# Kernel optimization log

Hardware: AMD Instinct MI355X
Metric: run time of the kernel (lower is better)

The kernel has to match this reference:

```python
import math
import jax, jax.numpy as jnp
import numpy as np

B, N, M, C, H, POS = 2, 2048, 64, 256, 8, 6
D = C // H  # head_dim = 32
SCALE = 1.0 / math.sqrt(D)
LAMDA = 1.0


def setup_inputs() -> dict:
    key = jax.random.key(0)
    ks = jax.random.split(key, 15)
    s = 0.05
    return {
        "pairwise_g": jax.random.normal(ks[0], (B, N, N, POS), jnp.float32),
        "coset_functions": jax.random.normal(ks[1], (B, N, C), jnp.float32),
        "mask": jnp.ones((B, N), dtype=bool),
        "Wq": jax.random.normal(ks[2], (C, C), jnp.float32) * s,
        "bq": jax.random.normal(ks[3], (C,), jnp.float32) * s,
        "Wk": jax.random.normal(ks[4], (C, C), jnp.float32) * s,
        "bk": jax.random.normal(ks[5], (C,), jnp.float32) * s,
        "Wl": jax.random.normal(ks[6], (C, POS), jnp.float32) * s,
        "bl": jax.random.normal(ks[7], (C,), jnp.float32) * s,
        "u": jax.random.normal(ks[8], (H, D), jnp.float32) * s,
        "v": jax.random.normal(ks[9], (H, D), jnp.float32) * s,
        "Wi": jax.random.normal(ks[10], (C, C), jnp.float32) * s,
        "bi": jax.random.normal(ks[11], (C,), jnp.float32) * s,
        "Wo": jax.random.normal(ks[12], (C, C), jnp.float32) * s,
        "bo": jax.random.normal(ks[13], (C,), jnp.float32) * s,
    }


def reference(pairwise_g, coset_functions, mask, Wq, bq, Wk, bk, Wl, bl, u, v, Wi, bi, Wo, bo):
    # ---- extract_neighbourhoods (mc_samples=M, fill=1.0 -> k == k_ball, permutation irrelevant)
    dists = jnp.linalg.norm(pairwise_g, axis=-1)                      # (B,N,N)
    dists = jnp.where(mask[:, None, :], dists, jnp.float32(1e8))
    _, nbhd_idx = jax.lax.top_k(-dists, M)                            # (B,N,M) nearest neighbors
    nbhd_pg = jnp.take_along_axis(pairwise_g, nbhd_idx[..., None], axis=2)  # (B,N,M,POS)
    gather_rows = jax.vmap(lambda arr, ix: arr[ix])                   # gather along point axis per batch
    nbhd_cf = gather_rows(coset_functions, nbhd_idx)                  # (B,N,M,C)
    nbhd_mask = gather_rows(mask, nbhd_idx)                           # (B,N,M)

    # ---- RelativePositionKernel
    Q = (coset_functions @ Wq.T + bq).reshape(B, N, H, D).transpose(0, 2, 1, 3)  # (B,H,N,D)
    K = (coset_functions @ Wk.T + bk).reshape(B, N, H, D).transpose(0, 2, 1, 3)  # (B,H,N,D)
    e = (nbhd_pg @ Wl.T + bl).reshape(B, N, M, H, D)                  # (B,N,M,H,D)

    S = jnp.einsum('bhnd,bhkd->bhnk', Q, K)                           # dense scores (as original)
    Sg = jnp.take_along_axis(S, nbhd_idx[:, None, :, :], axis=3)      # (B,H,N,M)
    e_term = jnp.einsum('bnmhd,bhnd->bhnm', e, Q + v[None, :, None, :])
    uK = jnp.einsum('hd,bhkd->bhk', u, K)                             # (B,H,N)
    uKg = jnp.take_along_axis(uK[:, :, None, :], nbhd_idx[:, None, :, :], axis=3)  # (B,H,N,M)
    A = (Sg + LAMDA * e_term + uKg) * SCALE
    A = A.transpose(0, 2, 3, 1)                                       # (B,N,M,H)

    # ---- masked softmax over neighbors
    A = jnp.where(nbhd_mask[..., None], A, jnp.float32(-1e38))
    attn = jax.nn.softmax(A, axis=2)                                  # (B,N,M,H)

    # ---- value projection + weighted sum + output linear
    Vv = (nbhd_cf @ Wi.T + bi).reshape(B, N, M, H, D)                 # (B,N,M,H,D)
    out = jnp.einsum('bnmh,bnmhd->bnhd', attn, Vv).reshape(B, N, C)
    out = out @ Wo.T + bo                                             # (B,N,c_out)
    return out
```

## Files before the change

kernel.cpp:

```cpp
#include <hip/hip_runtime.h>
#include <stdint.h>

#define NB 2
#define NN 2048
#define MM 64
#define CC 256
#define HH 8
#define DD 32
#define PP 6
#define ATT_SCALE 0.17677669529663687f

typedef __attribute__((ext_vector_type(8))) short short8;
typedef __attribute__((ext_vector_type(4))) float f32x4;

__device__ __forceinline__ uint16_t f2bf(float f) {
  union { float f; uint32_t u; } c; c.f = f;
  return (uint16_t)((c.u + 0x7fffu + ((c.u >> 16) & 1u)) >> 16);
}
__device__ __forceinline__ float blo(uint32_t u) {
  union { uint32_t u; float f; } c; c.u = u << 16; return c.f;
}
__device__ __forceinline__ float bhi(uint32_t u) {
  union { uint32_t u; float f; } c; c.u = u & 0xffff0000u; return c.f;
}
__device__ __forceinline__ short8 pack8(float4 a, float4 b) {
  short8 r;
  r[0] = (short)f2bf(a.x); r[1] = (short)f2bf(a.y);
  r[2] = (short)f2bf(a.z); r[3] = (short)f2bf(a.w);
  r[4] = (short)f2bf(b.x); r[5] = (short)f2bf(b.y);
  r[6] = (short)f2bf(b.z); r[7] = (short)f2bf(b.w);
  return r;
}

__global__ __launch_bounds__(256) void k_select(const float* __restrict__ pg,
                                                int* __restrict__ nidx) {
  const int row = blockIdx.x;
  const int t = threadIdx.x;
  const int wave = t >> 6;
  const int lane = t & 63;

  __shared__ float s_mn[4], s_mx[4];
  __shared__ uint32_t s_hist[256];
  __shared__ uint32_t s_scan[256];
  __shared__ float s_cd[NN];
  __shared__ int   s_cj[NN];
  __shared__ int s_tbin;
  __shared__ uint32_t s_c0;
  __shared__ int s_cw;
  __shared__ int s_ct;

  if (t < MM) nidx[(size_t)row * MM + t] = t;

  const float4* base = (const float4*)(pg + (size_t)row * NN * PP);

  float d[8];
  float mn = 3.4e38f, mx = -3.4e38f;
#pragma unroll
  for (int i = 0; i < 4; i++) {
    const int j0 = i * 512 + 2 * t;
    const float4 qa = base[(size_t)(j0 >> 1) * 3 + 0];
    const float4 qb = base[(size_t)(j0 >> 1) * 3 + 1];
    const float4 qc = base[(size_t)(j0 >> 1) * 3 + 2];
    float s0 = __fmul_rn(qa.x, qa.x);
    s0 = __fadd_rn(s0, __fmul_rn(qa.y, qa.y));
    s0 = __fadd_rn(s0, __fmul_rn(qa.z, qa.z));
    s0 = __fadd_rn(s0, __fmul_rn(qa.w, qa.w));
    s0 = __fadd_rn(s0, __fmul_rn(qb.x, qb.x));
    s0 = __fadd_rn(s0, __fmul_rn(qb.y, qb.y));
    float s1 = __fmul_rn(qb.z, qb.z);
    s1 = __fadd_rn(s1, __fmul_rn(qb.w, qb.w));
    s1 = __fadd_rn(s1, __fmul_rn(qc.x, qc.x));
    s1 = __fadd_rn(s1, __fmul_rn(qc.y, qc.y));
    s1 = __fadd_rn(s1, __fmul_rn(qc.z, qc.z));
    s1 = __fadd_rn(s1, __fmul_rn(qc.w, qc.w));
    const float d0 = __fsqrt_rn(s0);
    const float d1 = __fsqrt_rn(s1);
    d[2 * i] = d0; d[2 * i + 1] = d1;
    mn = fminf(mn, fminf(d0, d1));
    mx = fmaxf(mx, fmaxf(d0, d1));
  }

#pragma unroll
  for (int off = 32; off; off >>= 1) {
    mn = fminf(mn, __shfl_xor(mn, off));
    mx = fmaxf(mx, __shfl_xor(mx, off));
  }
  if (lane == 0) { s_mn[wave] = mn; s_mx[wave] = mx; }
  s_hist[t] = 0;
  __syncthreads();
  mn = fminf(fminf(s_mn[0], s_mn[1]), fminf(s_mn[2], s_mn[3]));
  mx = fmaxf(fmaxf(s_mx[0], s_mx[1]), fmaxf(s_mx[2], s_mx[3]));
  const float range = mx - mn;
  const float scale = (range > 0.f) ? (256.0f / range) : 0.f;

  int bins[8];
#pragma unroll
  for (int i = 0; i < 8; i++) {
    int bn = (int)((d[i] - mn) * scale);
    bn = (bn > 255) ? 255 : (bn < 0 ? 0 : bn);
    bins[i] = bn;
    atomicAdd(&s_hist[bn], 1u);
  }
  __syncthreads();

  s_scan[t] = s_hist[t];
  __syncthreads();
  for (int off = 1; off < 256; off <<= 1) {
    const uint32_t add = (t >= off) ? s_scan[t - off] : 0u;
    __syncthreads();
    s_scan[t] += add;
    __syncthreads();
  }

  if (t == 0) { s_cw = 0; s_ct = 0; }
  if (s_scan[t] >= (uint32_t)MM && (t == 0 || s_scan[t - 1] < (uint32_t)MM)) {
    s_tbin = t;
    s_c0 = (t == 0) ? 0u : s_scan[t - 1];
  }
  __syncthreads();

  const int tbin = s_tbin;
  const int c0 = (int)s_c0;

#pragma unroll
  for (int i = 0; i < 8; i++) {
    const int j = (i >> 1) * 512 + 2 * t + (i & 1);
    if (bins[i] < tbin) {
      const int pos = atomicAdd(&s_cw, 1);
      if (pos < MM) nidx[(size_t)row * MM + pos] = j;
    } else if (bins[i] == tbin) {
      const int pos = atomicAdd(&s_ct, 1);
      s_cd[pos] = d[i];
      s_cj[pos] = j;
    }
  }
  __syncthreads();

  if (t < 64) {
    const int cnt = s_ct;
    const int r = MM - c0;
    for (int it = 0; it < r; ++it) {
      float bd = 3.4e38f; int bj = 0x7fffffff; int bi = -1;
      for (int i = t; i < cnt; i += 64) {
        const float dd = s_cd[i]; const int jj = s_cj[i];
        if (dd < bd || (dd == bd && jj < bj)) { bd = dd; bj = jj; bi = i; }
      }
#pragma unroll
      for (int off = 32; off; off >>= 1) {
        const float od = __shfl_xor(bd, off);
        const int oj = __shfl_xor(bj, off);
        const int oi = __shfl_xor(bi, off);
        if (od < bd || (od == bd && oj < bj)) { bd = od; bj = oj; bi = oi; }
      }
      if (t == 0 && bi >= 0) {
        s_cd[bi] = 3.4e38f;
        nidx[(size_t)row * MM + c0 + it] = bj;
      }
      __threadfence_block();
    }
  }
}

__global__ __launch_bounds__(64) void k_gemm_qkv(
    const float* __restrict__ A,
    const float* __restrict__ W0, const float* __restrict__ W1, const float* __restrict__ W2,
    const float* __restrict__ b0, const float* __restrict__ b1, const float* __restrict__ b2,
    float* __restrict__ Qo, uint16_t* __restrict__ Ko, uint16_t* __restrict__ Vo) {
  const int z = blockIdx.z;
  const float* W = (z == 0) ? W0 : ((z == 1) ? W1 : W2);
  const float* bias = (z == 0) ? b0 : ((z == 1) ? b1 : b2);

  const int lane = threadIdx.x;
  const int m = lane & 15;
  const int quad = lane >> 4;
  const int row0 = blockIdx.x * 16;
  const int c0 = blockIdx.y * 64;

  f32x4 acc0 = {0.f, 0.f, 0.f, 0.f};
  f32x4 acc1 = {0.f, 0.f, 0.f, 0.f};
  f32x4 acc2 = {0.f, 0.f, 0.f, 0.f};
  f32x4 acc3 = {0.f, 0.f, 0.f, 0.f};

#pragma unroll
  for (int k0 = 0; k0 < CC; k0 += 32) {
    const float4* ap = (const float4*)(A + (size_t)(row0 + m) * CC + k0 + quad * 8);
    const float4* bp0 = (const float4*)(W + (size_t)(c0 + 0 + m) * CC + k0 + quad * 8);
    const float4* bp1 = (const float4*)(W + (size_t)(c0 + 16 + m) * CC + k0 + quad * 8);
    const float4* bp2 = (const float4*)(W + (size_t)(c0 + 32 + m) * CC + k0 + quad * 8);
    const float4* bp3 = (const float4*)(W + (size_t)(c0 + 48 + m) * CC + k0 + quad * 8);
    const short8 a = pack8(ap[0], ap[1]);
    const short8 f0 = pack8(bp0[0], bp0[1]);
    const short8 f1 = pack8(bp1[0], bp1[1]);
    const short8 f2 = pack8(bp2[0], bp2[1]);
    const short8 f3 = pack8(bp3[0], bp3[1]);
    acc0 = __builtin_amdgcn_mfma_f32_16x16x32_bf16(a, f0, acc0, 0, 0, 0);
    acc1 = __builtin_amdgcn_mfma_f32_16x16x32_bf16(a, f1, acc1, 0, 0, 0);
    acc2 = __builtin_amdgcn_mfma_f32_16x16x32_bf16(a, f2, acc2, 0, 0, 0);
    acc3 = __builtin_amdgcn_mfma_f32_16x16x32_bf16(a, f3, acc3, 0, 0, 0);
  }

  const int orow = row0 + quad * 4;
  f32x4 accs[4] = {acc0, acc1, acc2, acc3};
#pragma unroll
  for (int f = 0; f < 4; ++f) {
    const int col = c0 + f * 16 + m;
    const float bv = bias[col];
#pragma unroll
    for (int r = 0; r < 4; ++r) {
      const float val = accs[f][r] + bv;
      const size_t o = (size_t)(orow + r) * CC + col;
      if (z == 0) Qo[o] = val;
      else if (z == 1) Ko[o] = f2bf(val);
      else Vo[o] = f2bf(val);
    }
  }
}

__global__ __launch_bounds__(64) void k_gemm_out(const uint16_t* __restrict__ A,
                                                 const float* __restrict__ W,
                                                 const float* __restrict__ bias,
                                                 float* __restrict__ O) {
  const int lane = threadIdx.x;
  const int m = lane & 15;
  const int quad = lane >> 4;
  const int row0 = blockIdx.x * 16;
  const int c0 = blockIdx.y * 32;

  f32x4 acc0 = {0.f, 0.f, 0.f, 0.f};
  f32x4 acc1 = {0.f, 0.f, 0.f, 0.f};

#pragma unroll
  for (int k0 = 0; k0 < CC; k0 += 32) {
    const short8 a = *(const short8*)(A + (size_t)(row0 + m) * CC + k0 + quad * 8);
    const float4* bp0 = (const float4*)(W + (size_t)(c0 + 0 + m) * CC + k0 + quad * 8);
    const float4* bp1 = (const float4*)(W + (size_t)(c0 + 16 + m) * CC + k0 + quad * 8);
    const short8 f0 = pack8(bp0[0], bp0[1]);
    const short8 f1 = pack8(bp1[0], bp1[1]);
    acc0 = __builtin_amdgcn_mfma_f32_16x16x32_bf16(a, f0, acc0, 0, 0, 0);
    acc1 = __builtin_amdgcn_mfma_f32_16x16x32_bf16(a, f1, acc1, 0, 0, 0);
  }

  const int orow = row0 + quad * 4;
  f32x4 accs[2] = {acc0, acc1};
#pragma unroll
  for (int f = 0; f < 2; ++f) {
    const int col = c0 + f * 16 + m;
    const float bv = bias[col];
#pragma unroll
    for (int r = 0; r < 4; ++r) {
      O[(size_t)(orow + r) * CC + col] = accs[f][r] + bv;
    }
  }
}

__global__ __launch_bounds__(256) void k_attn(const float* __restrict__ pg,
                                              const int* __restrict__ nidx,
                                              const float* __restrict__ Q,
                                              const uint16_t* __restrict__ K,
                                              const uint16_t* __restrict__ V,
                                              const float* __restrict__ Wl,
                                              const float* __restrict__ bl,
                                              const float* __restrict__ u,
                                              const float* __restrict__ v,
                                              uint16_t* __restrict__ attnV) {
  const int row = blockIdx.x;
  const int b = row >> 11;
  const int t = threadIdx.x;
  const int wave = t >> 6;
  const int lane = t & 63;

  __shared__ int s_idx[MM];
  __shared__ float s_npg[MM][7];
  __shared__ float s_qu[CC];
  __shared__ float s_wt[HH][8];
  __shared__ float s_sc[HH][MM];
  __shared__ float s_part[CC];

  if (t < MM) s_idx[t] = nidx[(size_t)row * MM + t] & (NN - 1);
  const float qv_ = Q[(size_t)row * CC + t];
  s_qu[t] = qv_ + u[t];
  __syncthreads();

  if (t < MM) {
    const int jj = s_idx[t];
    const float2* p = (const float2*)(pg + ((size_t)row * NN + (size_t)jj) * PP);
    const float2 p0 = p[0], p1 = p[1], p2 = p[2];
    s_npg[t][0] = p0.x; s_npg[t][1] = p0.y;
    s_npg[t][2] = p1.x; s_npg[t][3] = p1.y;
    s_npg[t][4] = p2.x; s_npg[t][5] = p2.y;
  }

  {
    const int h = t >> 5;
    const float qpv = qv_ + v[t];
    float part[7];
#pragma unroll
    for (int p = 0; p < 6; p++) part[p] = Wl[(size_t)t * PP + p] * qpv;
    part[6] = bl[t] * qpv;
#pragma unroll
    for (int off = 1; off < 32; off <<= 1) {
#pragma unroll
      for (int p = 0; p < 7; p++) part[p] += __shfl_xor(part[p], off);
    }
    if ((t & 31) == 0) {
#pragma unroll
      for (int p = 0; p < 7; p++) s_wt[h][p] = part[p];
    }
  }
  __syncthreads();

#pragma unroll
  for (int pr = 0; pr < 2; ++pr) {
    const int h = wave + pr * 4;
    const int m = lane;
    const int kidx = s_idx[m];
    const uint4* kr = (const uint4*)(K + ((size_t)(b * NN + kidx)) * CC + h * DD);
    float acc = s_wt[h][6];
#pragma unroll
    for (int p = 0; p < 6; p++) acc += s_npg[m][p] * s_wt[h][p];
    const float* qu = &s_qu[h * DD];
    float a2 = 0.f;
#pragma unroll
    for (int w4 = 0; w4 < 4; w4++) {
      const uint4 kv = kr[w4];
      const float* q8 = qu + w4 * 8;
      a2 += q8[0] * blo(kv.x) + q8[1] * bhi(kv.x)
          + q8[2] * blo(kv.y) + q8[3] * bhi(kv.y)
          + q8[4] * blo(kv.z) + q8[5] * bhi(kv.z)
          + q8[6] * blo(kv.w) + q8[7] * bhi(kv.w);
    }
    s_sc[h][m] = (acc + a2) * ATT_SCALE;
  }
  __syncthreads();

#pragma unroll
  for (int pr = 0; pr < 2; ++pr) {
    const int h = wave + pr * 4;
    const float x = s_sc[h][lane];
    float mxv = x;
#pragma unroll
    for (int off = 32; off; off >>= 1) mxv = fmaxf(mxv, __shfl_xor(mxv, off));
    const float e = expf(x - mxv);
    float sm = e;
#pragma unroll
    for (int off = 32; off; off >>= 1) sm += __shfl_xor(sm, off);
    s_sc[h][lane] = e / sm;
  }
  __syncthreads();

  {
    const int h2 = t >> 7;
    const int ci = (t & 127) * 2;
    const int h = ci >> 5;
    const uint32_t* Vb32 = (const uint32_t*)(V + (size_t)b * NN * CC);
    float a0 = 0.f, a1 = 0.f;
#pragma unroll 8
    for (int m = h2; m < MM; m += 2) {
      const uint32_t pv = Vb32[(size_t)s_idx[m] * (CC / 2) + (ci >> 1)];
      const float p = s_sc[h][m];
      a0 += p * blo(pv);
      a1 += p * bhi(pv);
    }
    if (h2 == 1) { s_part[ci] = a0; s_part[ci + 1] = a1; }
    __syncthreads();
    if (h2 == 0) {
      attnV[(size_t)row * CC + ci]     = f2bf(a0 + s_part[ci]);
      attnV[(size_t)row * CC + ci + 1] = f2bf(a1 + s_part[ci + 1]);
    }
  }
}

extern "C" void kernel_launch(void* const* d_in, const int* in_sizes, int n_in,
                              void* d_out, int out_size, void* d_ws, size_t ws_size,
                              hipStream_t stream) {
  const float* pg = (const float*)d_in[0];
  const float* cf = (const float*)d_in[1];
  const float* Wq = (const float*)d_in[3];
  const float* bq = (const float*)d_in[4];
  const float* Wk = (const float*)d_in[5];
  const float* bk = (const float*)d_in[6];
  const float* Wl = (const float*)d_in[7];
  const float* bl = (const float*)d_in[8];
  const float* u  = (const float*)d_in[9];
  const float* v  = (const float*)d_in[10];
  const float* Wi = (const float*)d_in[11];
  const float* bi = (const float*)d_in[12];
  const float* Wo = (const float*)d_in[13];
  const float* bo = (const float*)d_in[14];

  char* ws = (char*)d_ws;
  int* nidx = (int*)ws;
  float* Q  = (float*)(ws + (size_t)1 * (1 << 20));
  uint16_t* K = (uint16_t*)(ws + (size_t)5 * (1 << 20));
  uint16_t* V = (uint16_t*)(ws + (size_t)7 * (1 << 20));
  uint16_t* aV = (uint16_t*)(ws + (size_t)9 * (1 << 20));
  float* out = (float*)d_out;

  hipLaunchKernelGGL(k_gemm_qkv, dim3(256, 4, 3), dim3(64), 0, stream,
                     cf, Wq, Wk, Wi, bq, bk, bi, Q, K, V);
  hipLaunchKernelGGL(k_select, dim3(NB * NN), dim3(256), 0, stream, pg, nidx);
  hipLaunchKernelGGL(k_attn, dim3(NB * NN), dim3(256), 0, stream,
                     pg, nidx, Q, K, V, Wl, bl, u, v, aV);
  hipLaunchKernelGGL(k_gemm_out, dim3(256, 8), dim3(64), 0, stream,
                     aV, Wo, bo, out);
}
```

Measured before the change: 384.1 us.

## Fuse neighbour selection into attention kernel and use wave-shuffle histogram scan

Merges the top-k neighbour selection kernel and the attention kernel into one per-row kernel, so neighbour indices stay in shared memory instead of being written to and re-read from global memory. This also removes one launch. The 256-bin histogram prefix sum is replaced by a wave-level shuffle scan plus a cross-wave add, which cuts the number of block barriers. The fused kernel uses more shared memory per block, which may reduce occupancy.

```diff
diff --git a/kernel.cpp b/kernel.cpp
--- a/kernel.cpp
+++ b/kernel.cpp
@@ -32,14 +32,115 @@
   return r;
 }
 
-__global__ __launch_bounds__(256) void k_select(const float* __restrict__ pg,
-                                                int* __restrict__ nidx) {
+__global__ __launch_bounds__(64) void k_gemm_qkv(
+    const float* __restrict__ A,
+    const float* __restrict__ W0, const float* __restrict__ W1, const float* __restrict__ W2,
+    const float* __restrict__ b0, const float* __restrict__ b1, const float* __restrict__ b2,
+    float* __restrict__ Qo, uint16_t* __restrict__ Ko, uint16_t* __restrict__ Vo) {
+  const int z = blockIdx.z;
+  const float* W = (z == 0) ? W0 : ((z == 1) ? W1 : W2);
+  const float* bias = (z == 0) ? b0 : ((z == 1) ? b1 : b2);
+
+  const int lane = threadIdx.x;
+  const int m = lane & 15;
+  const int quad = lane >> 4;
+  const int row0 = blockIdx.x * 16;
+  const int c0 = blockIdx.y * 64;
+
+  f32x4 acc0 = {0.f, 0.f, 0.f, 0.f};
+  f32x4 acc1 = {0.f, 0.f, 0.f, 0.f};
+  f32x4 acc2 = {0.f, 0.f, 0.f, 0.f};
+  f32x4 acc3 = {0.f, 0.f, 0.f, 0.f};
+
+#pragma unroll
+  for (int k0 = 0; k0 < CC; k0 += 32) {
+    const float4* ap = (const float4*)(A + (size_t)(row0 + m) * CC + k0 + quad * 8);
+    const float4* bp0 = (const float4*)(W + (size_t)(c0 + 0 + m) * CC + k0 + quad * 8);
+    const float4* bp1 = (const float4*)(W + (size_t)(c0 + 16 + m) * CC + k0 + quad * 8);
+    const float4* bp2 = (const float4*)(W + (size_t)(c0 + 32 + m) * CC + k0 + quad * 8);
+    const float4* bp3 = (const float4*)(W + (size_t)(c0 + 48 + m) * CC + k0 + quad * 8);
+    const short8 a = pack8(ap[0], ap[1]);
+    const short8 f0 = pack8(bp0[0], bp0[1]);
+    const short8 f1 = pack8(bp1[0], bp1[1]);
+    const short8 f2 = pack8(bp2[0], bp2[1]);
+    const short8 f3 = pack8(bp3[0], bp3[1]);
+    acc0 = __builtin_amdgcn_mfma_f32_16x16x32_bf16(a, f0, acc0, 0, 0, 0);
+    acc1 = __builtin_amdgcn_mfma_f32_16x16x32_bf16(a, f1, acc1, 0, 0, 0);
+    acc2 = __builtin_amdgcn_mfma_f32_16x16x32_bf16(a, f2, acc2, 0, 0, 0);
+    acc3 = __builtin_amdgcn_mfma_f32_16x16x32_bf16(a, f3, acc3, 0, 0, 0);
+  }
+
+  const int orow = row0 + quad * 4;
+  f32x4 accs[4] = {acc0, acc1, acc2, acc3};
+#pragma unroll
+  for (int f = 0; f < 4; ++f) {
+    const int col = c0 + f * 16 + m;
+    const float bv = bias[col];
+#pragma unroll
+    for (int r = 0; r < 4; ++r) {
+      const float val = accs[f][r] + bv;
+      const size_t o = (size_t)(orow + r) * CC + col;
+      if (z == 0) Qo[o] = val;
+      else if (z == 1) Ko[o] = f2bf(val);
+      else Vo[o] = f2bf(val);
+    }
+  }
+}
+
+__global__ __launch_bounds__(64) void k_gemm_out(const uint16_t* __restrict__ A,
+                                                 const float* __restrict__ W,
+                                                 const float* __restrict__ bias,
+                                                 float* __restrict__ O) {
+  const int lane = threadIdx.x;
+  const int m = lane & 15;
+  const int quad = lane >> 4;
+  const int row0 = blockIdx.x * 16;
+  const int c0 = blockIdx.y * 32;
+
+  f32x4 acc0 = {0.f, 0.f, 0.f, 0.f};
+  f32x4 acc1 = {0.f, 0.f, 0.f, 0.f};
+
+#pragma unroll
+  for (int k0 = 0; k0 < CC; k0 += 32) {
+    const short8 a = *(const short8*)(A + (size_t)(row0 + m) * CC + k0 + quad * 8);
+    const float4* bp0 = (const float4*)(W + (size_t)(c0 + 0 + m) * CC + k0 + quad * 8);
+    const float4* bp1 = (const float4*)(W + (size_t)(c0 + 16 + m) * CC + k0 + quad * 8);
+    const short8 f0 = pack8(bp0[0], bp0[1]);
+    const short8 f1 = pack8(bp1[0], bp1[1]);
+    acc0 = __builtin_amdgcn_mfma_f32_16x16x32_bf16(a, f0, acc0, 0, 0, 0);
+    acc1 = __builtin_amdgcn_mfma_f32_16x16x32_bf16(a, f1, acc1, 0, 0, 0);
+  }
+
+  const int orow = row0 + quad * 4;
+  f32x4 accs[2] = {acc0, acc1};
+#pragma unroll
+  for (int f = 0; f < 2; ++f) {
+    const int col = c0 + f * 16 + m;
+    const float bv = bias[col];
+#pragma unroll
+    for (int r = 0; r < 4; ++r) {
+      O[(size_t)(orow + r) * CC + col] = accs[f][r] + bv;
+    }
+  }
+}
+
+__global__ __launch_bounds__(256) void k_fused(const float* __restrict__ pg,
+                                               const float* __restrict__ Q,
+                                               const uint16_t* __restrict__ K,
+                                               const uint16_t* __restrict__ V,
+                                               const float* __restrict__ Wl,
+                                               const float* __restrict__ bl,
+                                               const float* __restrict__ u,
+                                               const float* __restrict__ v,
+                                               uint16_t* __restrict__ attnV) {
   const int row = blockIdx.x;
+  const int b = row >> 11;
   const int t = threadIdx.x;
   const int wave = t >> 6;
   const int lane = t & 63;
 
   __shared__ float s_mn[4], s_mx[4];
+  __shared__ uint32_t s_wsum[4];
   __shared__ uint32_t s_hist[256];
   __shared__ uint32_t s_scan[256];
   __shared__ float s_cd[NN];
@@ -48,8 +149,16 @@
   __shared__ uint32_t s_c0;
   __shared__ int s_cw;
   __shared__ int s_ct;
-
-  if (t < MM) nidx[(size_t)row * MM + t] = t;
+  __shared__ int s_idx[MM];
+  __shared__ float s_npg[MM][7];
+  __shared__ float s_qu[CC];
+  __shared__ float s_wt[HH][8];
+  __shared__ float s_sc[HH][MM];
+  __shared__ float s_part[CC];
+
+  const float qv_ = Q[(size_t)row * CC + t];
+  s_qu[t] = qv_ + u[t];
+  if (t < MM) s_idx[t] = t;
 
   const float4* base = (const float4*)(pg + (size_t)row * NN * PP);
 
@@ -103,16 +212,23 @@
   }
   __syncthreads();
 
-  s_scan[t] = s_hist[t];
-  __syncthreads();
-  for (int off = 1; off < 256; off <<= 1) {
-    const uint32_t add = (t >= off) ? s_scan[t - off] : 0u;
+  {
+    uint32_t x = s_hist[t];
+#pragma unroll
+    for (int off = 1; off < 64; off <<= 1) {
+      const uint32_t y = __shfl_up(x, off);
+      if (lane >= off) x += y;
+    }
+    if (lane == 63) s_wsum[wave] = x;
     __syncthreads();
-    s_scan[t] += add;
-    __syncthreads();
-  }
-
+    uint32_t pre = 0;
+    for (int w = 0; w < wave; w++) pre += s_wsum[w];
+    x += pre;
+    s_scan[t] = x;
+  }
   if (t == 0) { s_cw = 0; s_ct = 0; }
+  __syncthreads();
+
   if (s_scan[t] >= (uint32_t)MM && (t == 0 || s_scan[t - 1] < (uint32_t)MM)) {
     s_tbin = t;
     s_c0 = (t == 0) ? 0u : s_scan[t - 1];
@@ -127,7 +243,7 @@
     const int j = (i >> 1) * 512 + 2 * t + (i & 1);
     if (bins[i] < tbin) {
       const int pos = atomicAdd(&s_cw, 1);
-      if (pos < MM) nidx[(size_t)row * MM + pos] = j;
+      if (pos < MM) s_idx[pos] = j;
     } else if (bins[i] == tbin) {
       const int pos = atomicAdd(&s_ct, 1);
       s_cd[pos] = d[i];
@@ -154,135 +270,15 @@
       }
       if (t == 0 && bi >= 0) {
         s_cd[bi] = 3.4e38f;
-        nidx[(size_t)row * MM + c0 + it] = bj;
+        s_idx[c0 + it] = bj;
       }
       __threadfence_block();
     }
   }
-}
-
-__global__ __launch_bounds__(64) void k_gemm_qkv(
-    const float* __restrict__ A,
-    const float* __restrict__ W0, const float* __restrict__ W1, const float* __restrict__ W2,
-    const float* __restrict__ b0, const float* __restrict__ b1, const float* __restrict__ b2,
-    float* __restrict__ Qo, uint16_t* __restrict__ Ko, uint16_t* __restrict__ Vo) {
-  const int z = blockIdx.z;
-  const float* W = (z == 0) ? W0 : ((z == 1) ? W1 : W2);
-  const float* bias = (z == 0) ? b0 : ((z == 1) ? b1 : b2);
-
-  const int lane = threadIdx.x;
-  const int m = lane & 15;
-  const int quad = lane >> 4;
-  const int row0 = blockIdx.x * 16;
-  const int c0 = blockIdx.y * 64;
-
-  f32x4 acc0 = {0.f, 0.f, 0.f, 0.f};
-  f32x4 acc1 = {0.f, 0.f, 0.f, 0.f};
-  f32x4 acc2 = {0.f, 0.f, 0.f, 0.f};
-  f32x4 acc3 = {0.f, 0.f, 0.f, 0.f};
-
-#pragma unroll
-  for (int k0 = 0; k0 < CC; k0 += 32) {
-    const float4* ap = (const float4*)(A + (size_t)(row0 + m) * CC + k0 + quad * 8);
-    const float4* bp0 = (const float4*)(W + (size_t)(c0 + 0 + m) * CC + k0 + quad * 8);
-    const float4* bp1 = (const float4*)(W + (size_t)(c0 + 16 + m) * CC + k0 + quad * 8);
-    const float4* bp2 = (const float4*)(W + (size_t)(c0 + 32 + m) * CC + k0 + quad * 8);
-    const float4* bp3 = (const float4*)(W + (size_t)(c0 + 48 + m) * CC + k0 + quad * 8);
-    const short8 a = pack8(ap[0], ap[1]);
-    const short8 f0 = pack8(bp0[0], bp0[1]);
-    const short8 f1 = pack8(bp1[0], bp1[1]);
-    const short8 f2 = pack8(bp2[0], bp2[1]);
-    const short8 f3 = pack8(bp3[0], bp3[1]);
-    acc0 = __builtin_amdgcn_mfma_f32_16x16x32_bf16(a, f0, acc0, 0, 0, 0);
-    acc1 = __builtin_amdgcn_mfma_f32_16x16x32_bf16(a, f1, acc1, 0, 0, 0);
-    acc2 = __builtin_amdgcn_mfma_f32_16x16x32_bf16(a, f2, acc2, 0, 0, 0);
-    acc3 = __builtin_amdgcn_mfma_f32_16x16x32_bf16(a, f3, acc3, 0, 0, 0);
-  }
-
-  const int orow = row0 + quad * 4;
-  f32x4 accs[4] = {acc0, acc1, acc2, acc3};
-#pragma unroll
-  for (int f = 0; f < 4; ++f) {
-    const int col = c0 + f * 16 + m;
-    const float bv = bias[col];
-#pragma unroll
-    for (int r = 0; r < 4; ++r) {
-      const float val = accs[f][r] + bv;
-      const size_t o = (size_t)(orow + r) * CC + col;
-      if (z == 0) Qo[o] = val;
-      else if (z == 1) Ko[o] = f2bf(val);
-      else Vo[o] = f2bf(val);
-    }
-  }
-}
-
-__global__ __launch_bounds__(64) void k_gemm_out(const uint16_t* __restrict__ A,
-                                                 const float* __restrict__ W,
-                                                 const float* __restrict__ bias,
-                                                 float* __restrict__ O) {
-  const int lane = threadIdx.x;
-  const int m = lane & 15;
-  const int quad = lane >> 4;
-  const int row0 = blockIdx.x * 16;
-  const int c0 = blockIdx.y * 32;
-
-  f32x4 acc0 = {0.f, 0.f, 0.f, 0.f};
-  f32x4 acc1 = {0.f, 0.f, 0.f, 0.f};
-
-#pragma unroll
-  for (int k0 = 0; k0 < CC; k0 += 32) {
-    const short8 a = *(const short8*)(A + (size_t)(row0 + m) * CC + k0 + quad * 8);
-    const float4* bp0 = (const float4*)(W + (size_t)(c0 + 0 + m) * CC + k0 + quad * 8);
-    const float4* bp1 = (const float4*)(W + (size_t)(c0 + 16 + m) * CC + k0 + quad * 8);
-    const short8 f0 = pack8(bp0[0], bp0[1]);
-    const short8 f1 = pack8(bp1[0], bp1[1]);
-    acc0 = __builtin_amdgcn_mfma_f32_16x16x32_bf16(a, f0, acc0, 0, 0, 0);
-    acc1 = __builtin_amdgcn_mfma_f32_16x16x32_bf16(a, f1, acc1, 0, 0, 0);
-  }
-
-  const int orow = row0 + quad * 4;
-  f32x4 accs[2] = {acc0, acc1};
-#pragma unroll
-  for (int f = 0; f < 2; ++f) {
-    const int col = c0 + f * 16 + m;
-    const float bv = bias[col];
-#pragma unroll
-    for (int r = 0; r < 4; ++r) {
-      O[(size_t)(orow + r) * CC + col] = accs[f][r] + bv;
-    }
-  }
-}
-
-__global__ __launch_bounds__(256) void k_attn(const float* __restrict__ pg,
-                                              const int* __restrict__ nidx,
-                                              const float* __restrict__ Q,
-                                              const uint16_t* __restrict__ K,
-                                              const uint16_t* __restrict__ V,
-                                              const float* __restrict__ Wl,
-                                              const float* __restrict__ bl,
-                                              const float* __restrict__ u,
-                                              const float* __restrict__ v,
-                                              uint16_t* __restrict__ attnV) {
-  const int row = blockIdx.x;
-  const int b = row >> 11;
-  const int t = threadIdx.x;
-  const int wave = t >> 6;
-  const int lane = t & 63;
-
-  __shared__ int s_idx[MM];
-  __shared__ float s_npg[MM][7];
-  __shared__ float s_qu[CC];
-  __shared__ float s_wt[HH][8];
-  __shared__ float s_sc[HH][MM];
-  __shared__ float s_part[CC];
-
-  if (t < MM) s_idx[t] = nidx[(size_t)row * MM + t] & (NN - 1);
-  const float qv_ = Q[(size_t)row * CC + t];
-  s_qu[t] = qv_ + u[t];
   __syncthreads();
 
   if (t < MM) {
-    const int jj = s_idx[t];
+    const int jj = s_idx[t] & (NN - 1);
     const float2* p = (const float2*)(pg + ((size_t)row * NN + (size_t)jj) * PP);
     const float2 p0 = p[0], p1 = p[1], p2 = p[2];
     s_npg[t][0] = p0.x; s_npg[t][1] = p0.y;
@@ -313,7 +309,7 @@
   for (int pr = 0; pr < 2; ++pr) {
     const int h = wave + pr * 4;
     const int m = lane;
-    const int kidx = s_idx[m];
+    const int kidx = s_idx[m] & (NN - 1);
     const uint4* kr = (const uint4*)(K + ((size_t)(b * NN + kidx)) * CC + h * DD);
     float acc = s_wt[h][6];
 #pragma unroll
@@ -356,7 +352,7 @@
     float a0 = 0.f, a1 = 0.f;
 #pragma unroll 8
     for (int m = h2; m < MM; m += 2) {
-      const uint32_t pv = Vb32[(size_t)s_idx[m] * (CC / 2) + (ci >> 1)];
+      const uint32_t pv = Vb32[(size_t)(s_idx[m] & (NN - 1)) * (CC / 2) + (ci >> 1)];
       const float p = s_sc[h][m];
       a0 += p * blo(pv);
       a1 += p * bhi(pv);
@@ -389,18 +385,16 @@
   const float* bo = (const float*)d_in[14];
 
   char* ws = (char*)d_ws;
-  int* nidx = (int*)ws;
-  float* Q  = (float*)(ws + (size_t)1 * (1 << 20));
-  uint16_t* K = (uint16_t*)(ws + (size_t)5 * (1 << 20));
-  uint16_t* V = (uint16_t*)(ws + (size_t)7 * (1 << 20));
-  uint16_t* aV = (uint16_t*)(ws + (size_t)9 * (1 << 20));
+  float* Q  = (float*)ws;
+  uint16_t* K = (uint16_t*)(ws + (size_t)4 * (1 << 20));
+  uint16_t* V = (uint16_t*)(ws + (size_t)6 * (1 << 20));
+  uint16_t* aV = (uint16_t*)(ws + (size_t)8 * (1 << 20));
   float* out = (float*)d_out;
 
   hipLaunchKernelGGL(k_gemm_qkv, dim3(256, 4, 3), dim3(64), 0, stream,
                      cf, Wq, Wk, Wi, bq, bk, bi, Q, K, V);
-  hipLaunchKernelGGL(k_select, dim3(NB * NN), dim3(256), 0, stream, pg, nidx);
-  hipLaunchKernelGGL(k_attn, dim3(NB * NN), dim3(256), 0, stream,
-                     pg, nidx, Q, K, V, Wl, bl, u, v, aV);
+  hipLaunchKernelGGL(k_fused, dim3(NB * NN), dim3(256), 0, stream,
+                     pg, Q, K, V, Wl, bl, u, v, aV);
   hipLaunchKernelGGL(k_gemm_out, dim3(256, 8), dim3(64), 0, stream,
                      aV, Wo, bo, out);
 }
```

After: 359.0 us. 6.5% less time.
